# Optimization experiments

Measured on AMD Instinct MI355X. Metric: run time of the kernel, lower is better.

The kernel has to match this reference:

```python
import jax, jax.numpy as jnp
import numpy as np

D = 1024
M = 256
BATCH = 2048


def setup_inputs() -> dict:
    key = jax.random.key(0)
    kx, kw, kp = jax.random.split(key, 3)
    x = jax.random.uniform(kx, (BATCH, D), dtype=jnp.float32)
    W = jax.random.normal(kw, (M,), dtype=jnp.float32)
    P = jax.random.normal(kp, (M, D), dtype=jnp.float32)
    return {"x": x, "W": W, "P": P}


def reference(x, W, P):
    # log mixture weights: log softmax over m
    logw = jax.nn.log_softmax(W, axis=-1)              # [m]
    p = jax.nn.sigmoid(P)                              # [m, d]
    # broadcast Bernoulli likelihood: [batch, m, d]
    lik = x[:, None, :] * p[None, :, :] + (1.0 - x[:, None, :]) * (1.0 - p[None, :, :])
    # per-component log-likelihood summed over features, plus log weight
    comp_ll = jnp.sum(jnp.log(lik), axis=-1) + logw[None, :]   # [batch, m]
    # mixture log-likelihood via logsumexp over components
    return jax.scipy.special.logsumexp(comp_ll, axis=-1)       # [batch]
```

## Files before the change

### kernel.cpp

```cpp
#include <hip/hip_runtime.h>

#define BATCH 2048
#define MM    256
#define DD    1024

#define BB 128
#define BM 64
#define KC 16
#define TB 8
#define TM 4
#define LXS (BB + 4)
#define LRS (BM + 4)
#define NBT (BATCH / BB)

#define LOG2E 1.4426950408889634f
#define LN2   0.6931471805599453f

__device__ __forceinline__ float fr_mant(float x) {
#if __has_builtin(__builtin_amdgcn_frexp_mantf)
    return __builtin_amdgcn_frexp_mantf(x);
#else
    unsigned u = __float_as_uint(x);
    return __uint_as_float((u & 0x807FFFFFu) | 0x3F000000u);
#endif
}
__device__ __forceinline__ int fr_exp(float x) {
#if __has_builtin(__builtin_amdgcn_frexp_expf)
    return __builtin_amdgcn_frexp_expf(x);
#else
    return (int)((__float_as_uint(x) >> 23) & 0xFFu) - 126;
#endif
}

__global__ __launch_bounds__(256) void precomp_kernel(
        const float* __restrict__ P, const float* __restrict__ Wv,
        float* __restrict__ rbuf, float* __restrict__ cst) {
    const int m = blockIdx.x;
    const int t = threadIdx.x;
    const int lane = t & 63, wid = t >> 6;

    float4 z = ((const float4*)(P + (size_t)m * DD))[t];
    float e0 = __expf(z.x), e1 = __expf(z.y), e2 = __expf(z.z), e3 = __expf(z.w);
    ((float4*)(rbuf + (size_t)m * DD))[t] =
        make_float4(e0 - 1.f, e1 - 1.f, e2 - 1.f, e3 - 1.f);
    float part = -(__log2f(1.f + e0) + __log2f(1.f + e1) +
                   __log2f(1.f + e2) + __log2f(1.f + e3));

    __shared__ float smA[4], smB[4];

    #pragma unroll
    for (int o = 32; o; o >>= 1) part += __shfl_xor(part, o);
    if (lane == 0) smA[wid] = part;

    float w = Wv[t];
    float mx = w;
    #pragma unroll
    for (int o = 32; o; o >>= 1) mx = fmaxf(mx, __shfl_xor(mx, o));
    if (lane == 0) smB[wid] = mx;
    __syncthreads();

    float rowc = smA[0] + smA[1] + smA[2] + smA[3];
    float gmx  = fmaxf(fmaxf(smB[0], smB[1]), fmaxf(smB[2], smB[3]));

    float se = __expf(w - gmx);
    #pragma unroll
    for (int o = 32; o; o >>= 1) se += __shfl_xor(se, o);
    __syncthreads();
    if (lane == 0) smA[wid] = se;
    __syncthreads();

    if (t == 0) {
        float sum = smA[0] + smA[1] + smA[2] + smA[3];
        cst[m] = rowc + (Wv[m] - gmx) * LOG2E - __log2f(sum);
    }
}

__global__ __launch_bounds__(256, 4) void main_kernel(
        const float* __restrict__ x, const float* __restrict__ rbuf,
        float* __restrict__ pbuf, int dc) {
    __shared__ __align__(16) float lx[KC * LXS];
    __shared__ __align__(16) float lr[KC * LRS];

    const int tid = threadIdx.x;
    const int tx = tid & 15;
    const int ty = tid >> 4;

    const int gid  = blockIdx.x;
    const int xcd  = gid & 7;
    const int k    = gid >> 3;
    const int m_id = k & 3;
    const int tile = (k >> 2) * 8 + xcd;
    const int b_id = tile & (NBT - 1);
    const int d_id = tile / NBT;

    const int m0 = m_id * BM;
    const int b0 = b_id * BB;
    const int d0 = d_id * dc;
    const int NC = dc / KC;

    const int rowx = tid >> 2, segx = tid & 3;
    const float* xp0 = x + (size_t)(b0 + rowx) * DD + d0 + segx * 4;
    const float* xp1 = xp0 + (size_t)64 * DD;
    const float* rp  = rbuf + (size_t)(m0 + rowx) * DD + d0 + segx * 4;

    float4 cx0 = *(const float4*)xp0;
    float4 cx1 = *(const float4*)xp1;
    float4 cr  = *(const float4*)rp;

    float prod[TB][TM];
    int   acce[TB][TM];
    #pragma unroll
    for (int i = 0; i < TB; ++i)
        #pragma unroll
        for (int j = 0; j < TM; ++j) { prod[i][j] = 1.0f; acce[i][j] = 0; }

    for (int c = 0; c < NC; ++c) {
        __syncthreads();
        {
            const int base = segx * 4;
            lx[(base + 0) * LXS + rowx] = cx0.x;
            lx[(base + 1) * LXS + rowx] = cx0.y;
            lx[(base + 2) * LXS + rowx] = cx0.z;
            lx[(base + 3) * LXS + rowx] = cx0.w;
            lx[(base + 0) * LXS + rowx + 64] = cx1.x;
            lx[(base + 1) * LXS + rowx + 64] = cx1.y;
            lx[(base + 2) * LXS + rowx + 64] = cx1.z;
            lx[(base + 3) * LXS + rowx + 64] = cx1.w;
            if (rowx < BM) {
                lr[(base + 0) * LRS + rowx] = cr.x;
                lr[(base + 1) * LRS + rowx] = cr.y;
                lr[(base + 2) * LRS + rowx] = cr.z;
                lr[(base + 3) * LRS + rowx] = cr.w;
            }
        }
        if (c + 1 < NC) {
            xp0 += KC; xp1 += KC; rp += KC;
            cx0 = *(const float4*)xp0;
            cx1 = *(const float4*)xp1;
            cr  = *(const float4*)rp;
        }
        __syncthreads();

        #pragma unroll
        for (int kc = 0; kc < KC; ++kc) {
            const float4* xp = (const float4*)&lx[kc * LXS + TB * ty];
            float4 xa = xp[0], xb = xp[1];
            const float4* rpf = (const float4*)&lr[kc * LRS + TM * tx];
            float4 rv = rpf[0];
            float xf[TB] = {xa.x, xa.y, xa.z, xa.w, xb.x, xb.y, xb.z, xb.w};
            float rf[TM] = {rv.x, rv.y, rv.z, rv.w};
            #pragma unroll
            for (int i = 0; i < TB; ++i)
                #pragma unroll
                for (int j = 0; j < TM; ++j)
                    prod[i][j] *= fmaf(xf[i], rf[j], 1.0f);
        }
        #pragma unroll
        for (int i = 0; i < TB; ++i)
            #pragma unroll
            for (int j = 0; j < TM; ++j) {
                float p = prod[i][j];
                acce[i][j] += fr_exp(p);
                prod[i][j] = fr_mant(p);
            }
    }

    float* pb = pbuf + ((size_t)d_id * BATCH + b0) * MM + m0;
    #pragma unroll
    for (int i = 0; i < TB; ++i) {
        float4 vv;
        vv.x = (float)acce[i][0] + __log2f(prod[i][0]);
        vv.y = (float)acce[i][1] + __log2f(prod[i][1]);
        vv.z = (float)acce[i][2] + __log2f(prod[i][2]);
        vv.w = (float)acce[i][3] + __log2f(prod[i][3]);
        *(float4*)&pb[(size_t)(TB * ty + i) * MM + TM * tx] = vv;
    }
}

__global__ __launch_bounds__(256) void finalize16_kernel(
        const float4* __restrict__ pbuf4, const float4* __restrict__ cst4,
        float* __restrict__ out) {
    const int lane = threadIdx.x & 63;
    const int w = threadIdx.x >> 6;
    const int b = blockIdx.x * 4 + w;

    float4 v = cst4[lane];
    const float4* pb = pbuf4 + (size_t)b * (MM / 4) + lane;
    #pragma unroll
    for (int s = 0; s < 16; ++s) {
        float4 t = pb[(size_t)s * BATCH * (MM / 4)];
        v.x += t.x; v.y += t.y; v.z += t.z; v.w += t.w;
    }

    float mx = fmaxf(fmaxf(v.x, v.y), fmaxf(v.z, v.w));
    #pragma unroll
    for (int o = 32; o; o >>= 1) mx = fmaxf(mx, __shfl_xor(mx, o));

    float s = exp2f(v.x - mx) + exp2f(v.y - mx) + exp2f(v.z - mx) + exp2f(v.w - mx);
    #pragma unroll
    for (int o = 32; o; o >>= 1) s += __shfl_xor(s, o);

    if (lane == 0) out[b] = LN2 * (mx + __log2f(s));
}

__global__ __launch_bounds__(256) void finalize_kernel(
        const float* __restrict__ pbuf, const float* __restrict__ cst,
        float* __restrict__ out, int sd) {
    const int lane = threadIdx.x & 63;
    const int w = threadIdx.x >> 6;
    const int b = blockIdx.x * 4 + w;

    float v0 = cst[lane];
    float v1 = cst[lane + 64];
    float v2 = cst[lane + 128];
    float v3 = cst[lane + 192];

    for (int s = 0; s < sd; ++s) {
        const float* row = pbuf + ((size_t)s * BATCH + b) * MM;
        v0 += row[lane];
        v1 += row[lane + 64];
        v2 += row[lane + 128];
        v3 += row[lane + 192];
    }

    float mx = fmaxf(fmaxf(v0, v1), fmaxf(v2, v3));
    #pragma unroll
    for (int o = 32; o; o >>= 1) mx = fmaxf(mx, __shfl_xor(mx, o));

    float s = exp2f(v0 - mx) + exp2f(v1 - mx) + exp2f(v2 - mx) + exp2f(v3 - mx);
    #pragma unroll
    for (int o = 32; o; o >>= 1) s += __shfl_xor(s, o);

    if (lane == 0) out[b] = LN2 * (mx + __log2f(s));
}

extern "C" void kernel_launch(void* const* d_in, const int* in_sizes, int n_in,
                              void* d_out, int out_size, void* d_ws, size_t ws_size,
                              hipStream_t stream) {
    const float* x  = (const float*)d_in[0];
    const float* Wv = (const float*)d_in[1];
    const float* P  = (const float*)d_in[2];

    float* ws   = (float*)d_ws;
    float* rbuf = ws;
    float* cst  = rbuf + (size_t)MM * DD;
    float* pbuf = cst + MM;

    size_t fixed = ((size_t)MM * DD + MM) * sizeof(float);
    size_t avail = (ws_size > fixed) ? (ws_size - fixed) : 0;
    int sd = 16;
    while (sd > 1 && (size_t)sd * BATCH * MM * sizeof(float) > avail) sd >>= 1;

    precomp_kernel<<<MM, 256, 0, stream>>>(P, Wv, rbuf, cst);
    int nblocks = NBT * sd * 4;
    main_kernel<<<nblocks, 256, 0, stream>>>(x, rbuf, pbuf, DD / sd);
    if (sd == 16)
        finalize16_kernel<<<BATCH / 4, 256, 0, stream>>>(
            (const float4*)pbuf, (const float4*)cst, (float*)d_out);
    else
        finalize_kernel<<<BATCH / 4, 256, 0, stream>>>(pbuf, cst, (float*)d_out, sd);
}
```

Before: 92.48 us.

## Fuse precompute, main and finalize into one cooperative kernel with grid syncs

```diff
diff --git a/kernel.cpp b/kernel.cpp
--- a/kernel.cpp
+++ b/kernel.cpp
@@ -1,4 +1,7 @@
 #include <hip/hip_runtime.h>
+#include <hip/hip_cooperative_groups.h>
+
+namespace cg = cooperative_groups;
 
 #define BATCH 2048
 #define MM    256
@@ -12,6 +15,8 @@
 #define LXS (BB + 4)
 #define LRS (BM + 4)
 #define NBT (BATCH / BB)
+#define SD16 16
+#define DC16 (DD / SD16)
 
 #define LOG2E 1.4426950408889634f
 #define LN2   0.6931471805599453f
@@ -32,11 +37,11 @@
 #endif
 }
 
-__global__ __launch_bounds__(256) void precomp_kernel(
+
+__device__ __forceinline__ void precomp_body(
         const float* __restrict__ P, const float* __restrict__ Wv,
-        float* __restrict__ rbuf, float* __restrict__ cst) {
-    const int m = blockIdx.x;
-    const int t = threadIdx.x;
+        float* __restrict__ rbuf, float* __restrict__ cst,
+        int m, int t, float* smA, float* smB) {
     const int lane = t & 63, wid = t >> 6;
 
     float4 z = ((const float4*)(P + (size_t)m * DD))[t];
@@ -46,8 +51,6 @@
     float part = -(__log2f(1.f + e0) + __log2f(1.f + e1) +
                    __log2f(1.f + e2) + __log2f(1.f + e3));
 
-    __shared__ float smA[4], smB[4];
-
     #pragma unroll
     for (int o = 32; o; o >>= 1) part += __shfl_xor(part, o);
     if (lane == 0) smA[wid] = part;
@@ -75,17 +78,13 @@
     }
 }
 
-__global__ __launch_bounds__(256, 4) void main_kernel(
+__device__ __forceinline__ void main_body(
         const float* __restrict__ x, const float* __restrict__ rbuf,
-        float* __restrict__ pbuf, int dc) {
-    __shared__ __align__(16) float lx[KC * LXS];
-    __shared__ __align__(16) float lr[KC * LRS];
-
-    const int tid = threadIdx.x;
+        float* __restrict__ pbuf, int dc, int gid, int tid,
+        float* lx, float* lr) {
     const int tx = tid & 15;
     const int ty = tid >> 4;
 
-    const int gid  = blockIdx.x;
     const int xcd  = gid & 7;
     const int k    = gid >> 3;
     const int m_id = k & 3;
@@ -177,30 +176,73 @@
     }
 }
 
+__device__ __forceinline__ void finalize16_body(
+        const float4* __restrict__ pbuf4, const float4* __restrict__ cst4,
+        float* __restrict__ out, int b, int lane) {
+    float4 v = cst4[lane];
+    const float4* pb = pbuf4 + (size_t)b * (MM / 4) + lane;
+    #pragma unroll
+    for (int s = 0; s < 16; ++s) {
+        float4 t = pb[(size_t)s * BATCH * (MM / 4)];
+        v.x += t.x; v.y += t.y; v.z += t.z; v.w += t.w;
+    }
+
+    float mx = fmaxf(fmaxf(v.x, v.y), fmaxf(v.z, v.w));
+    #pragma unroll
+    for (int o = 32; o; o >>= 1) mx = fmaxf(mx, __shfl_xor(mx, o));
+
+    float s = exp2f(v.x - mx) + exp2f(v.y - mx) + exp2f(v.z - mx) + exp2f(v.w - mx);
+    #pragma unroll
+    for (int o = 32; o; o >>= 1) s += __shfl_xor(s, o);
+
+    if (lane == 0) out[b] = LN2 * (mx + __log2f(s));
+}
+
+__global__ __launch_bounds__(256, 4) void fused_kernel(
+        const float* __restrict__ x, const float* __restrict__ Wv,
+        const float* __restrict__ P, float* __restrict__ rbuf,
+        float* __restrict__ cst, float* __restrict__ pbuf,
+        float* __restrict__ out) {
+    __shared__ __align__(16) float lx[KC * LXS];
+    __shared__ __align__(16) float lr[KC * LRS];
+    __shared__ float smA[4], smB[4];
+
+    cg::grid_group grid = cg::this_grid();
+    const int tid = threadIdx.x;
+
+    if (blockIdx.x < MM)
+        precomp_body(P, Wv, rbuf, cst, blockIdx.x, tid, smA, smB);
+    grid.sync();
+
+    main_body(x, rbuf, pbuf, DC16, blockIdx.x, tid, lx, lr);
+    grid.sync();
+
+    const int w = tid >> 6;
+    if (w < 2)
+        finalize16_body((const float4*)pbuf, (const float4*)cst, out,
+                        blockIdx.x * 2 + w, tid & 63);
+}
+
+__global__ __launch_bounds__(256) void precomp_kernel(
+        const float* __restrict__ P, const float* __restrict__ Wv,
+        float* __restrict__ rbuf, float* __restrict__ cst) {
+    __shared__ float smA[4], smB[4];
+    precomp_body(P, Wv, rbuf, cst, blockIdx.x, threadIdx.x, smA, smB);
+}
+
+__global__ __launch_bounds__(256, 4) void main_kernel(
+        const float* __restrict__ x, const float* __restrict__ rbuf,
+        float* __restrict__ pbuf, int dc) {
+    __shared__ __align__(16) float lx[KC * LXS];
+    __shared__ __align__(16) float lr[KC * LRS];
+    main_body(x, rbuf, pbuf, dc, blockIdx.x, threadIdx.x, lx, lr);
+}
+
 __global__ __launch_bounds__(256) void finalize16_kernel(
         const float4* __restrict__ pbuf4, const float4* __restrict__ cst4,
         float* __restrict__ out) {
-    const int lane = threadIdx.x & 63;
     const int w = threadIdx.x >> 6;
-    const int b = blockIdx.x * 4 + w;
-
-    float4 v = cst4[lane];
-    const float4* pb = pbuf4 + (size_t)b * (MM / 4) + lane;
-    #pragma unroll
-    for (int s = 0; s < 16; ++s) {
-        float4 t = pb[(size_t)s * BATCH * (MM / 4)];
-        v.x += t.x; v.y += t.y; v.z += t.z; v.w += t.w;
-    }
-
-    float mx = fmaxf(fmaxf(v.x, v.y), fmaxf(v.z, v.w));
-    #pragma unroll
-    for (int o = 32; o; o >>= 1) mx = fmaxf(mx, __shfl_xor(mx, o));
-
-    float s = exp2f(v.x - mx) + exp2f(v.y - mx) + exp2f(v.z - mx) + exp2f(v.w - mx);
-    #pragma unroll
-    for (int o = 32; o; o >>= 1) s += __shfl_xor(s, o);
-
-    if (lane == 0) out[b] = LN2 * (mx + __log2f(s));
+    finalize16_body(pbuf4, cst4, out, blockIdx.x * 4 + w, threadIdx.x & 63);
 }
 
 __global__ __launch_bounds__(256) void finalize_kernel(
@@ -245,11 +287,22 @@
     float* rbuf = ws;
     float* cst  = rbuf + (size_t)MM * DD;
     float* pbuf = cst + MM;
+    float* outp = (float*)d_out;
 
     size_t fixed = ((size_t)MM * DD + MM) * sizeof(float);
     size_t avail = (ws_size > fixed) ? (ws_size - fixed) : 0;
     int sd = 16;
     while (sd > 1 && (size_t)sd * BATCH * MM * sizeof(float) > avail) sd >>= 1;
+
+    if (sd == 16) {
+        void* args[] = {(void*)&x, (void*)&Wv, (void*)&P, (void*)&rbuf,
+                        (void*)&cst, (void*)&pbuf, (void*)&outp};
+        hipError_t e = hipLaunchCooperativeKernel(
+            (const void*)fused_kernel, dim3(NBT * SD16 * 4), dim3(256),
+            args, 0, stream);
+        if (e == hipSuccess) return;
+        (void)hipGetLastError();
+    }
 
     precomp_kernel<<<MM, 256, 0, stream>>>(P, Wv, rbuf, cst);
     int nblocks = NBT * sd * 4;
```

Measured after the change: 339.8 us. +267.4%, slower.
